# Performance work log

Hardware: AMD Instinct MI355X
Metric: run time of the kernel (lower is better)

Reference implementation:

```python
import jax, jax.numpy as jnp
import numpy as np

HEADS = 4
DIM_HEAD = 32
DIM = 128
B, N, Hq, Wg = 2, 6, 32, 32   # batch, cameras, BEV grid
HK, WK = 28, 60               # image feature map


def _ln(x, g, b, eps=1e-5):
    mu = jnp.mean(x, axis=-1, keepdims=True)
    var = jnp.mean((x - mu) ** 2, axis=-1, keepdims=True)
    return (x - mu) * jax.lax.rsqrt(var + eps) * g + b


def setup_inputs() -> dict:
    key = jax.random.key(0)
    ks = jax.random.split(key, 12)
    s = 0.05  # weight scale to keep softmax logits well-conditioned
    inp = {
        'q': jax.random.normal(ks[0], (B, N, DIM, Hq, Wg), jnp.float32),
        'k': jax.random.normal(ks[1], (B, N, DIM, HK, WK), jnp.float32),
        'v': jax.random.normal(ks[2], (B, N, DIM, HK, WK), jnp.float32),
        'skip': jax.random.normal(ks[3], (B, DIM, Hq, Wg), jnp.float32),
        'q_ln_g': jnp.ones((DIM,), jnp.float32),
        'q_ln_b': jnp.zeros((DIM,), jnp.float32),
        'Wq': s * jax.random.normal(ks[4], (DIM, HEADS * DIM_HEAD), jnp.float32),
        'bq': jnp.zeros((HEADS * DIM_HEAD,), jnp.float32),
        'k_ln_g': jnp.ones((DIM,), jnp.float32),
        'k_ln_b': jnp.zeros((DIM,), jnp.float32),
        'Wk': s * jax.random.normal(ks[5], (DIM, HEADS * DIM_HEAD), jnp.float32),
        'bk': jnp.zeros((HEADS * DIM_HEAD,), jnp.float32),
        'v_ln_g': jnp.ones((DIM,), jnp.float32),
        'v_ln_b': jnp.zeros((DIM,), jnp.float32),
        'Wv': s * jax.random.normal(ks[6], (DIM, HEADS * DIM_HEAD), jnp.float32),
        'bv': jnp.zeros((HEADS * DIM_HEAD,), jnp.float32),
        'Wp': s * jax.random.normal(ks[7], (HEADS * DIM_HEAD, DIM), jnp.float32),
        'bp': jnp.zeros((DIM,), jnp.float32),
        'pre_g': jnp.ones((DIM,), jnp.float32),
        'pre_b': jnp.zeros((DIM,), jnp.float32),
        'W1': s * jax.random.normal(ks[8], (DIM, 2 * DIM), jnp.float32),
        'b1': jnp.zeros((2 * DIM,), jnp.float32),
        'W2': s * jax.random.normal(ks[9], (2 * DIM, DIM), jnp.float32),
        'b2': jnp.zeros((DIM,), jnp.float32),
        'post_g': jnp.ones((DIM,), jnp.float32),
        'post_b': jnp.zeros((DIM,), jnp.float32),
    }
    return inp


def reference(q, k, v, skip, q_ln_g, q_ln_b, Wq, bq, k_ln_g, k_ln_b, Wk, bk,
              v_ln_g, v_ln_b, Wv, bv, Wp, bp, pre_g, pre_b,
              W1, b1, W2, b2, post_g, post_b):
    b, n, d, H, W = q.shape
    Q = H * W
    K = k.shape[3] * k.shape[4]
    m, dh = HEADS, DIM_HEAD
    # b n d H W -> b n Q d   /  b n d h w -> b n K d  /  b (n K) d
    qf = q.transpose(0, 1, 3, 4, 2).reshape(b, n, Q, d)
    kf = k.transpose(0, 1, 3, 4, 2).reshape(b, n, K, d)
    vf = v.transpose(0, 1, 3, 4, 2).reshape(b, n * K, d)
    # norm -> linear, then split heads: b ... (m dh) -> (b m) ... dh
    qh = (_ln(qf, q_ln_g, q_ln_b) @ Wq + bq).reshape(b, n, Q, m, dh)
    qh = qh.transpose(0, 3, 1, 2, 4).reshape(b * m, n, Q, dh)
    kh = (_ln(kf, k_ln_g, k_ln_b) @ Wk + bk).reshape(b, n, K, m, dh)
    kh = kh.transpose(0, 3, 1, 2, 4).reshape(b * m, n, K, dh)
    vh = (_ln(vf, v_ln_g, v_ln_b) @ Wv + bv).reshape(b, n * K, m, dh)
    vh = vh.transpose(0, 2, 1, 3).reshape(b * m, n * K, dh)
    scale = dh ** -0.5
    dot = scale * jnp.einsum('anqd,ankd->anqk', qh, kh)   # (b m) n Q K
    dot = dot.transpose(0, 2, 1, 3).reshape(b * m, Q, n * K)  # fold views into keys
    att = jax.nn.softmax(dot, axis=-1)
    a = jnp.einsum('aqk,akd->aqd', att, vh)               # (b m) Q dh
    a = a.reshape(b, m, Q, dh).transpose(0, 2, 1, 3).reshape(b, Q, m * dh)
    z = a @ Wp + bp
    z = z + skip.transpose(0, 2, 3, 1).reshape(b, Q, d)
    z = _ln(z, pre_g, pre_b)
    z = z + (jax.nn.gelu(z @ W1 + b1, approximate=False) @ W2 + b2)
    z = _ln(z, post_g, post_b)
    return z.reshape(b, H, W, d).transpose(0, 3, 1, 2)
```

## Files before the change

kernel.cpp:

```cpp
#include <hip/hip_runtime.h>
#include <math.h>

#define NCAM 6
#define BSZ 2
#define SQL 1024
#define SKL 1680
#define NHEAD 4
#define DHEAD 32
#define QSCALE 0.25503494f

typedef unsigned short ushort_t;
typedef unsigned int uint_t;
typedef __attribute__((ext_vector_type(8))) short short8;
typedef __attribute__((ext_vector_type(4))) float f32x4;

#define MFMA16 __builtin_amdgcn_mfma_f32_16x16x32_bf16

__device__ __forceinline__ ushort_t f2bf(float x) {
  uint_t u = __builtin_bit_cast(uint_t, x);
  u += 0x7FFFu + ((u >> 16) & 1u);
  return (ushort_t)(u >> 16);
}

__device__ __forceinline__ float fast_gelu(float x) {
  const float ax = fabsf(x) * 0.70710678118654752f;
  const float tt = __builtin_amdgcn_rcpf(fmaf(0.3275911f, ax, 1.f));
  float poly = fmaf(tt, 1.061405429f, -1.453152027f);
  poly = fmaf(tt, poly, 1.421413741f);
  poly = fmaf(tt, poly, -0.284496736f);
  poly = fmaf(tt, poly, 0.254829592f);
  poly *= tt;
  const float e = __builtin_amdgcn_exp2f(-ax * ax * 1.4426950408889634f);
  float er = fmaf(-poly, e, 1.f);
  er = copysignf(er, x);
  return 0.5f * x * (1.f + er);
}

__global__ __launch_bounds__(256) void prep_kernel(
    const float* __restrict__ Wq, const float* __restrict__ qg, const float* __restrict__ qb, const float* __restrict__ bq,
    const float* __restrict__ Wk, const float* __restrict__ kg, const float* __restrict__ kbb, const float* __restrict__ bk,
    const float* __restrict__ Wv, const float* __restrict__ vg, const float* __restrict__ vbb, const float* __restrict__ bv,
    const float* __restrict__ Wp,
    const float* __restrict__ W1, const float* __restrict__ pre_g, const float* __restrict__ pre_b, const float* __restrict__ b1,
    const float* __restrict__ W2,
    ushort_t* WqT, ushort_t* WkT, ushort_t* WvT, ushort_t* WpT, ushort_t* W1T, ushort_t* W2T,
    float* uq, float* bbq, float* uk, float* bbk, float* uv, float* bbv, float* b1p) {
  const int mb = blockIdx.x;
  const float *W, *g = nullptr, *bln = nullptr, *bias = nullptr;
  ushort_t* WT; float *u = nullptr, *bb = nullptr;
  int kin = 128, nout = 128, ob;
  if (mb < 4)       { W=Wq; g=qg; bln=qb;   bias=bq; WT=WqT; u=uq; bb=bbq; ob=mb*32; }
  else if (mb < 8)  { W=Wk; g=kg; bln=kbb;  bias=bk; WT=WkT; u=uk; bb=bbk; ob=(mb-4)*32; }
  else if (mb < 12) { W=Wv; g=vg; bln=vbb;  bias=bv; WT=WvT; u=uv; bb=bbv; ob=(mb-8)*32; }
  else if (mb < 16) { W=Wp; WT=WpT; ob=(mb-12)*32; }
  else if (mb < 24) { W=W1; g=pre_g; bln=pre_b; bias=b1; WT=W1T; bb=b1p; nout=256; ob=(mb-16)*32; }
  else              { W=W2; WT=W2T; kin=256; ob=(mb-24)*32; }
  const int t = threadIdx.x;
  const int oc = t & 31, ig = t >> 5;
  const int out = ob + oc;
  const int nper = kin >> 3;
  float su = 0.f, sb = 0.f;
  for (int j0 = 0; j0 < nper; j0 += 8) {
    float wv8[8];
#pragma unroll
    for (int j = 0; j < 8; ++j)
      wv8[j] = W[(size_t)(ig * nper + j0 + j) * nout + out];
#pragma unroll
    for (int j = 0; j < 8; ++j) {
      const int in = ig * nper + j0 + j;
      const float wg = g ? g[in] * wv8[j] : wv8[j];
      WT[(size_t)out * kin + in] = f2bf(wg);
      su += wg;
      if (bln) sb += bln[in] * wv8[j];
    }
  }
  __shared__ float sU[8][32], sB[8][32];
  sU[ig][oc] = su; sB[ig][oc] = sb;
  __syncthreads();
  if (t < 32) {
    float tu = 0.f, tb = 0.f;
#pragma unroll
    for (int i = 0; i < 8; ++i) { tu += sU[i][t]; tb += sB[i][t]; }
    if (u)  u[ob + t] = tu;
    if (bb) bb[ob + t] = tb + (bias ? bias[ob + t] : 0.f);
  }
}

__global__ __launch_bounds__(256) void proj_mfma(
    const float* __restrict__ xq, const float* __restrict__ xk, const float* __restrict__ xv,
    const ushort_t* __restrict__ WqT, const ushort_t* __restrict__ WkT, const ushort_t* __restrict__ WvT,
    const float* __restrict__ uq, const float* __restrict__ uk, const float* __restrict__ uv,
    const float* __restrict__ bbq, const float* __restrict__ bbk, const float* __restrict__ bbv,
    ushort_t* __restrict__ Qh, ushort_t* __restrict__ Kh, ushort_t* __restrict__ Vt) {
  int blk = blockIdx.x;
  const float* x; const ushort_t* WT; const float* u; const float* bb;
  ushort_t* out; int S, ntile, vmode; float oscale;
  if (blk < 192)      { x=xq; WT=WqT; u=uq; bb=bbq; out=Qh; S=SQL; ntile=16; vmode=0; oscale=QSCALE; }
  else if (blk < 516) { blk-=192; x=xk; WT=WkT; u=uk; bb=bbk; out=Kh; S=SKL; ntile=27; vmode=0; oscale=1.f; }
  else                { blk-=516; x=xv; WT=WvT; u=uv; bb=bbv; out=Vt; S=SKL; ntile=27; vmode=1; oscale=1.f; }
  const int bn = blk / ntile;
  const int pos0 = (blk - bn * ntile) * 64;
  int valid = S - pos0; if (valid > 64) valid = 64;

  const int t = threadIdx.x;
  __shared__ ushort_t sX[64 * 128];
  __shared__ float sS1[16][64], sS2[16][64];
  __shared__ float sMu[64], sRs[64];

  {
    const int posq = t & 15, chg = t >> 4;
    int lp4 = 4 * posq; if (lp4 >= valid) lp4 = valid - 4;
    const float* xb = x + ((size_t)bn * 128 + chg * 8) * S + pos0 + lp4;
    float v[8][4];
#pragma unroll
    for (int i = 0; i < 8; ++i) {
      const float4 f = *((const float4*)(xb + (size_t)i * S));
      v[i][0] = f.x; v[i][1] = f.y; v[i][2] = f.z; v[i][3] = f.w;
    }
#pragma unroll
    for (int j = 0; j < 4; ++j) {
      float s1 = 0.f, s2 = 0.f;
#pragma unroll
      for (int i = 0; i < 8; ++i) { s1 += v[i][j]; s2 += v[i][j] * v[i][j]; }
      sS1[chg][lp4 + j] = s1; sS2[chg][lp4 + j] = s2;
    }
#pragma unroll
    for (int j = 0; j < 4; ++j) {
      const int pos = lp4 + j;
      short8 pk;
#pragma unroll
      for (int i = 0; i < 8; ++i) pk[i] = (short)f2bf(v[i][j]);
      const int phys = chg ^ (pos & 7);
      *((short8*)&sX[pos * 128 + phys * 8]) = pk;
    }
  }
  __syncthreads();
  if (t < 64) {
    float a1 = 0.f, a2 = 0.f;
#pragma unroll
    for (int g = 0; g < 16; ++g) { a1 += sS1[g][t]; a2 += sS2[g][t]; }
    const float mu = a1 * (1.f / 128.f);
    sMu[t] = mu; sRs[t] = rsqrtf(a2 * (1.f / 128.f) - mu * mu + 1e-5f);
  }
  __syncthreads();

  const int w = t >> 6, l = t & 63, lq = l & 15, quad = l >> 4;
  short8 af[2][4];
#pragma unroll
  for (int ms = 0; ms < 2; ++ms)
#pragma unroll
    for (int kk = 0; kk < 4; ++kk)
      af[ms][kk] = *((const short8*)(WT + (size_t)(w * 32 + ms * 16 + lq) * 128 + quad * 8 + kk * 32));
  f32x4 acc[4][2];
#pragma unroll
  for (int ns = 0; ns < 4; ++ns)
#pragma unroll
    for (int ms = 0; ms < 2; ++ms) acc[ns][ms] = (f32x4){0.f, 0.f, 0.f, 0.f};
#pragma unroll
  for (int ns = 0; ns < 4; ++ns) {
    short8 bf[4];
#pragma unroll
    for (int kk = 0; kk < 4; ++kk) {
      const int phys = (quad + 4 * kk) ^ (lq & 7);
      bf[kk] = *((const short8*)&sX[(ns * 16 + lq) * 128 + phys * 8]);
    }
#pragma unroll
    for (int ms = 0; ms < 2; ++ms) {
      f32x4 a = acc[ns][ms];
#pragma unroll
      for (int kk = 0; kk < 4; ++kk) a = MFMA16(af[ms][kk], bf[kk], a, 0, 0, 0);
      acc[ns][ms] = a;
    }
  }

  const int b_ = bn / NCAM, cam = bn - b_ * NCAM;
  const size_t slab = (size_t)((b_ * NHEAD + w) * NCAM + cam);
#pragma unroll
  for (int ms = 0; ms < 2; ++ms) {
    float uu[4], bv_[4];
#pragma unroll
    for (int r = 0; r < 4; ++r) {
      const int og = w * 32 + ms * 16 + quad * 4 + r;
      uu[r] = u[og]; bv_[r] = bb[og];
    }
#pragma unroll
    for (int ns = 0; ns < 4; ++ns) {
      const int p = ns * 16 + lq;
      if (p < valid) {
        const float mu = sMu[p], rs = sRs[p];
        float val[4];
#pragma unroll
        for (int r = 0; r < 4; ++r)
          val[r] = ((acc[ns][ms][r] - mu * uu[r]) * rs + bv_[r]) * oscale;
        if (vmode == 0) {
          ushort_t e0 = f2bf(val[0]), e1 = f2bf(val[1]), e2 = f2bf(val[2]), e3 = f2bf(val[3]);
          ushort_t* orow = out + (slab * S + pos0 + p) * 32 + ms * 16 + quad * 4;
          *((uint_t*)orow) = (uint_t)e0 | ((uint_t)e1 << 16);
          *((uint_t*)(orow + 2)) = (uint_t)e2 | ((uint_t)e3 << 16);
        } else {
#pragma unroll
          for (int r = 0; r < 4; ++r)
            out[(slab * 32 + ms * 16 + quad * 4 + r) * (size_t)SKL + pos0 + p] = f2bf(val[r]);
        }
      }
    }
  }
}

__global__ __launch_bounds__(512, 2) void attn_mfma(
    const ushort_t* __restrict__ Qh, const ushort_t* __restrict__ Kh,
    const ushort_t* __restrict__ Vt, ushort_t* __restrict__ Ab) {
  const int t = threadIdx.x;
  const int w = t >> 6, l = t & 63;
  const int lq = l & 15, quad = l >> 4;
  const int bm = blockIdx.x & 7;
  const int q0 = (blockIdx.x >> 3) * 32;
  const int camg = w >> 2, kq = w & 3;
  const int kstart = kq * 448;
  const int nfull = (kq == 3) ? 5 : 7;

  __shared__ __align__(16) unsigned char smem[74752];
  ushort_t (*sP)[2][16][72] = (ushort_t(*)[2][16][72])smem;
  float (*sO)[2][16][36] = (float(*)[2][16][36])smem;
  float (*sL)[2][16] = (float(*)[2][16])(smem + 73728);

  f32x4 oA0 = {0.f,0.f,0.f,0.f}, oA1 = {0.f,0.f,0.f,0.f};
  f32x4 oB0 = {0.f,0.f,0.f,0.f}, oB1 = {0.f,0.f,0.f,0.f};
  float lA = 0.f, lB = 0.f;

  for (int nc = 0; nc < 3; ++nc) {
    const int n = camg * 3 + nc;
    const ushort_t* Kb = Kh + (size_t)(bm * NCAM + n) * SKL * 32;
    const ushort_t* Vb = Vt + (size_t)(bm * NCAM + n) * 32 * SKL;
    const ushort_t* Qbase = Qh + ((size_t)(bm * NCAM + n) * SQL + q0) * 32;
    const short8 qfA = *((const short8*)(Qbase + (size_t)lq * 32 + quad * 8));
    const short8 qfB = *((const short8*)(Qbase + (size_t)(16 + lq) * 32 + quad * 8));

    short8 kc[4];
#pragma unroll
    for (int st = 0; st < 4; ++st)
      kc[st] = *((const short8*)(Kb + (size_t)(kstart + st * 16 + lq) * 32 + quad * 8));

    for (int kt = 0; kt < nfull; ++kt) {
      const int kb = kstart + kt * 64;
      const short8 v00 = *((const short8*)(Vb + (size_t)lq * SKL + kb + quad * 8));
      const short8 v01 = *((const short8*)(Vb + (size_t)lq * SKL + kb + 32 + quad * 8));
      const short8 v10 = *((const short8*)(Vb + (size_t)(16 + lq) * SKL + kb + quad * 8));
      const short8 v11 = *((const short8*)(Vb + (size_t)(16 + lq) * SKL + kb + 32 + quad * 8));
      short8 kn[4] = {kc[0], kc[1], kc[2], kc[3]};
      if (kt + 1 < nfull) {
        const int kbn = kb + 64;
#pragma unroll
        for (int st = 0; st < 4; ++st)
          kn[st] = *((const short8*)(Kb + (size_t)(kbn + st * 16 + lq) * 32 + quad * 8));
      }

      f32x4 sA[4], sB[4];
#pragma unroll
      for (int st = 0; st < 4; ++st) {
        f32x4 z = {0.f, 0.f, 0.f, 0.f};
        sA[st] = MFMA16(kc[st], qfA, z, 0, 0, 0);
        sB[st] = MFMA16(kc[st], qfB, z, 0, 0, 0);
      }
      float lsA = 0.f, lsB = 0.f;
#pragma unroll
      for (int st = 0; st < 4; ++st) {
        const float a0 = __builtin_amdgcn_exp2f(sA[st][0]);
        const float a1 = __builtin_amdgcn_exp2f(sA[st][1]);
        const float a2 = __builtin_amdgcn_exp2f(sA[st][2]);
        const float a3 = __builtin_amdgcn_exp2f(sA[st][3]);
        const float b0 = __builtin_amdgcn_exp2f(sB[st][0]);
        const float b1 = __builtin_amdgcn_exp2f(sB[st][1]);
        const float b2 = __builtin_amdgcn_exp2f(sB[st][2]);
        const float b3 = __builtin_amdgcn_exp2f(sB[st][3]);
        lsA += (a0 + a1) + (a2 + a3);
        lsB += (b0 + b1) + (b2 + b3);
        const uint_t pa0 = __builtin_amdgcn_perm(__builtin_bit_cast(uint_t, a1), __builtin_bit_cast(uint_t, a0), 0x07060302u);
        const uint_t pa1 = __builtin_amdgcn_perm(__builtin_bit_cast(uint_t, a3), __builtin_bit_cast(uint_t, a2), 0x07060302u);
        const uint_t pb0 = __builtin_amdgcn_perm(__builtin_bit_cast(uint_t, b1), __builtin_bit_cast(uint_t, b0), 0x07060302u);
        const uint_t pb1 = __builtin_amdgcn_perm(__builtin_bit_cast(uint_t, b3), __builtin_bit_cast(uint_t, b2), 0x07060302u);
        *((uint2*)&sP[w][0][lq][st * 16 + quad * 4]) = make_uint2(pa0, pa1);
        *((uint2*)&sP[w][1][lq][st * 16 + quad * 4]) = make_uint2(pb0, pb1);
      }
      const short8 pfA0 = *((const short8*)&sP[w][0][lq][quad * 8]);
      const short8 pfA1 = *((const short8*)&sP[w][0][lq][32 + quad * 8]);
      const short8 pfB0 = *((const short8*)&sP[w][1][lq][quad * 8]);
      const short8 pfB1 = *((const short8*)&sP[w][1][lq][32 + quad * 8]);
      oA0 = MFMA16(v00, pfA0, oA0, 0, 0, 0);
      oA1 = MFMA16(v10, pfA0, oA1, 0, 0, 0);
      oB0 = MFMA16(v00, pfB0, oB0, 0, 0, 0);
      oB1 = MFMA16(v10, pfB0, oB1, 0, 0, 0);
      oA0 = MFMA16(v01, pfA1, oA0, 0, 0, 0);
      oA1 = MFMA16(v11, pfA1, oA1, 0, 0, 0);
      oB0 = MFMA16(v01, pfB1, oB0, 0, 0, 0);
      oB1 = MFMA16(v11, pfB1, oB1, 0, 0, 0);
      lsA += __shfl_xor(lsA, 16, 64);
      lsA += __shfl_xor(lsA, 32, 64);
      lsB += __shfl_xor(lsB, 16, 64);
      lsB += __shfl_xor(lsB, 32, 64);
      lA += lsA; lB += lsB;
#pragma unroll
      for (int st = 0; st < 4; ++st) kc[st] = kn[st];
    }

    if (kq == 3) {
      const int kb = kstart + 320;
      const short8 kf = *((const short8*)(Kb + (size_t)(kb + lq) * 32 + quad * 8));
      const short8 v00 = *((const short8*)(Vb + (size_t)lq * SKL + kb + quad * 8));
      const short8 v10 = *((const short8*)(Vb + (size_t)(16 + lq) * SKL + kb + quad * 8));
      f32x4 z = {0.f, 0.f, 0.f, 0.f};
      const f32x4 s0A = MFMA16(kf, qfA, z, 0, 0, 0);
      const f32x4 s0B = MFMA16(kf, qfB, z, 0, 0, 0);
      const float a0 = __builtin_amdgcn_exp2f(s0A[0]);
      const float a1 = __builtin_amdgcn_exp2f(s0A[1]);
      const float a2 = __builtin_amdgcn_exp2f(s0A[2]);
      const float a3 = __builtin_amdgcn_exp2f(s0A[3]);
      const float b0 = __builtin_amdgcn_exp2f(s0B[0]);
      const float b1 = __builtin_amdgcn_exp2f(s0B[1]);
      const float b2 = __builtin_amdgcn_exp2f(s0B[2]);
      const float b3 = __builtin_amdgcn_exp2f(s0B[3]);
      float lsA = (a0 + a1) + (a2 + a3);
      float lsB = (b0 + b1) + (b2 + b3);
      const uint_t pa0 = __builtin_amdgcn_perm(__builtin_bit_cast(uint_t, a1), __builtin_bit_cast(uint_t, a0), 0x07060302u);
      const uint_t pa1 = __builtin_amdgcn_perm(__builtin_bit_cast(uint_t, a3), __builtin_bit_cast(uint_t, a2), 0x07060302u);
      const uint_t pb0 = __builtin_amdgcn_perm(__builtin_bit_cast(uint_t, b1), __builtin_bit_cast(uint_t, b0), 0x07060302u);
      const uint_t pb1 = __builtin_amdgcn_perm(__builtin_bit_cast(uint_t, b3), __builtin_bit_cast(uint_t, b2), 0x07060302u);
      *((uint2*)&sP[w][0][lq][quad * 4]) = make_uint2(pa0, pa1);
      *((uint2*)&sP[w][0][lq][16 + quad * 4]) = make_uint2(0u, 0u);
      *((uint2*)&sP[w][1][lq][quad * 4]) = make_uint2(pb0, pb1);
      *((uint2*)&sP[w][1][lq][16 + quad * 4]) = make_uint2(0u, 0u);
      const short8 pfA0 = *((const short8*)&sP[w][0][lq][quad * 8]);
      const short8 pfB0 = *((const short8*)&sP[w][1][lq][quad * 8]);
      oA0 = MFMA16(v00, pfA0, oA0, 0, 0, 0);
      oA1 = MFMA16(v10, pfA0, oA1, 0, 0, 0);
      oB0 = MFMA16(v00, pfB0, oB0, 0, 0, 0);
      oB1 = MFMA16(v10, pfB0, oB1, 0, 0, 0);
      lsA += __shfl_xor(lsA, 16, 64);
      lsA += __shfl_xor(lsA, 32, 64);
      lsB += __shfl_xor(lsB, 16, 64);
      lsB += __shfl_xor(lsB, 32, 64);
      lA += lsA; lB += lsB;
    }
  }

  __syncthreads();
  *((f32x4*)&sO[w][0][lq][quad * 4]) = oA0;
  *((f32x4*)&sO[w][0][lq][16 + quad * 4]) = oA1;
  *((f32x4*)&sO[w][1][lq][quad * 4]) = oB0;
  *((f32x4*)&sO[w][1][lq][16 + quad * 4]) = oB1;
  if (l < 16) { sL[w][0][l] = lA; sL[w][1][l] = lB; }
  __syncthreads();
  if (w < 2) {
    const int frag = w;
    float lf = 0.f;
    f32x4 a0 = {0.f, 0.f, 0.f, 0.f}, a1 = {0.f, 0.f, 0.f, 0.f};
#pragma unroll
    for (int ww = 0; ww < 8; ++ww) {
      lf += sL[ww][frag][lq];
      a0 += *((const f32x4*)&sO[ww][frag][lq][quad * 4]);
      a1 += *((const f32x4*)&sO[ww][frag][lq][16 + quad * 4]);
    }
    const float inv = 1.f / lf;
    const int b = bm >> 2, hm = bm & 3;
    ushort_t* op = Ab + ((size_t)b * SQL + q0 + frag * 16 + lq) * 128 + hm * 32 + quad * 4;
    ushort4 w0 = make_ushort4(f2bf(a0[0] * inv), f2bf(a0[1] * inv), f2bf(a0[2] * inv), f2bf(a0[3] * inv));
    ushort4 w1 = make_ushort4(f2bf(a1[0] * inv), f2bf(a1[1] * inv), f2bf(a1[2] * inv), f2bf(a1[3] * inv));
    *((ushort4*)op) = w0;
    *((ushort4*)(op + 16)) = w1;
  }
}

__global__ __launch_bounds__(256) void post_mfma(
    const ushort_t* __restrict__ Ab, const float* __restrict__ skip,
    const ushort_t* __restrict__ WpT, const float* __restrict__ bp,
    const float* __restrict__ pre_g, const float* __restrict__ pre_b,
    const ushort_t* __restrict__ W1T, const float* __restrict__ b1p,
    const ushort_t* __restrict__ W2T, const float* __restrict__ b2,
    const float* __restrict__ post_g, const float* __restrict__ post_b,
    float* __restrict__ out) {
  const int t = threadIdx.x;
  const int w = t >> 6, l = t & 63, lq = l & 15, quad = l >> 4;
  const int b = blockIdx.x >> 7;
  const int p0 = (blockIdx.x & 127) * 8;
  const int rp = (p0 + lq < SQL) ? (p0 + lq) : (SQL - 1);

  __shared__ float zf[16 * 132];
  __shared__ float sRes[16 * 132];
  __shared__ ushort_t sZb[16 * 128];
  __shared__ ushort_t sH[16 * 256];
  __shared__ float sMu[16], sRs[16];

  f32x4 z[2] = {{0.f,0.f,0.f,0.f},{0.f,0.f,0.f,0.f}};
#pragma unroll
  for (int kk = 0; kk < 4; ++kk) {
    const short8 bfr = *((const short8*)(Ab + ((size_t)b * SQL + rp) * 128 + quad * 8 + kk * 32));
#pragma unroll
    for (int ms = 0; ms < 2; ++ms) {
      const short8 afr = *((const short8*)(WpT + (size_t)(w * 32 + ms * 16 + lq) * 128 + quad * 8 + kk * 32));
      z[ms] = MFMA16(afr, bfr, z[ms], 0, 0, 0);
    }
  }
#pragma unroll
  for (int ms = 0; ms < 2; ++ms)
#pragma unroll
    for (int r = 0; r < 4; ++r) {
      const int o = w * 32 + ms * 16 + quad * 4 + r;
      const int rr = (p0 + lq < SQL) ? (p0 + lq) : (SQL - 1);
      zf[lq * 132 + o] = z[ms][r] + bp[o] + skip[(size_t)b * 131072 + (size_t)o * 1024 + rr];
    }
  __syncthreads();
  {
    const int pos = t >> 4, j = t & 15;
    float s1 = 0.f, s2 = 0.f;
#pragma unroll
    for (int c = 0; c < 8; ++c) { const float vv = zf[pos * 132 + j * 8 + c]; s1 += vv; s2 += vv * vv; }
    s1 += __shfl_xor(s1, 1, 64); s1 += __shfl_xor(s1, 2, 64);
    s1 += __shfl_xor(s1, 4, 64); s1 += __shfl_xor(s1, 8, 64);
    s2 += __shfl_xor(s2, 1, 64); s2 += __shfl_xor(s2, 2, 64);
    s2 += __shfl_xor(s2, 4, 64); s2 += __shfl_xor(s2, 8, 64);
    if (j == 0) {
      const float mu = s1 * (1.f / 128.f);
      sMu[pos] = mu; sRs[pos] = rsqrtf(s2 * (1.f / 128.f) - mu * mu + 1e-5f);
    }
  }
  __syncthreads();
  {
    const int pos = t & 15, grp = t >> 4;
    const float mu = sMu[pos], rs = sRs[pos];
    short8 pk;
#pragma unroll
    for (int i = 0; i < 8; ++i) {
      const int ch = grp * 8 + i;
      const float nv = (zf[pos * 132 + ch] - mu) * rs;
      pk[i] = (short)f2bf(nv);
      sRes[pos * 132 + ch] = nv * pre_g[ch] + pre_b[ch];
    }
    *((short8*)&sZb[pos * 128 + (grp ^ (pos & 7)) * 8]) = pk;
  }
  __syncthreads();
  f32x4 h[4];
#pragma unroll
  for (int ms = 0; ms < 4; ++ms) h[ms] = (f32x4){0.f, 0.f, 0.f, 0.f};
  short8 bz[4];
#pragma unroll
  for (int kk = 0; kk < 4; ++kk)
    bz[kk] = *((const short8*)&sZb[lq * 128 + ((quad + 4 * kk) ^ (lq & 7)) * 8]);
#pragma unroll
  for (int ms = 0; ms < 4; ++ms)
#pragma unroll
    for (int kk = 0; kk < 4; ++kk) {
      const short8 afr = *((const short8*)(W1T + (size_t)(w * 64 + ms * 16 + lq) * 128 + quad * 8 + kk * 32));
      h[ms] = MFMA16(afr, bz[kk], h[ms], 0, 0, 0);
    }
#pragma unroll
  for (int ms = 0; ms < 4; ++ms)
#pragma unroll
    for (int r = 0; r < 4; ++r) {
      const int o = w * 64 + ms * 16 + quad * 4 + r;
      const float hv = fast_gelu(h[ms][r] + b1p[o]);
      const int phys = (o >> 3) ^ (lq & 7);
      sH[lq * 256 + phys * 8 + (o & 7)] = f2bf(hv);
    }
  __syncthreads();
  f32x4 z2[2] = {{0.f,0.f,0.f,0.f},{0.f,0.f,0.f,0.f}};
#pragma unroll
  for (int kk = 0; kk < 8; ++kk) {
    const short8 bh = *((const short8*)&sH[lq * 256 + ((quad + 4 * kk) ^ (lq & 7)) * 8]);
#pragma unroll
    for (int ms = 0; ms < 2; ++ms) {
      const short8 afr = *((const short8*)(W2T + (size_t)(w * 32 + ms * 16 + lq) * 256 + quad * 8 + kk * 32));
      z2[ms] = MFMA16(afr, bh, z2[ms], 0, 0, 0);
    }
  }
  __syncthreads();
#pragma unroll
  for (int ms = 0; ms < 2; ++ms)
#pragma unroll
    for (int r = 0; r < 4; ++r) {
      const int o = w * 32 + ms * 16 + quad * 4 + r;
      zf[lq * 132 + o] = z2[ms][r] + b2[o] + sRes[lq * 132 + o];
    }
  __syncthreads();
  {
    const int pos = t >> 4, j = t & 15;
    float s1 = 0.f, s2 = 0.f;
#pragma unroll
    for (int c = 0; c < 8; ++c) { const float vv = zf[pos * 132 + j * 8 + c]; s1 += vv; s2 += vv * vv; }
    s1 += __shfl_xor(s1, 1, 64); s1 += __shfl_xor(s1, 2, 64);
    s1 += __shfl_xor(s1, 4, 64); s1 += __shfl_xor(s1, 8, 64);
    s2 += __shfl_xor(s2, 1, 64); s2 += __shfl_xor(s2, 2, 64);
    s2 += __shfl_xor(s2, 4, 64); s2 += __shfl_xor(s2, 8, 64);
    if (j == 0) {
      const float mu = s1 * (1.f / 128.f);
      sMu[pos] = mu; sRs[pos] = rsqrtf(s2 * (1.f / 128.f) - mu * mu + 1e-5f);
    }
  }
  __syncthreads();
  {
    const int pos = t & 15, grp = t >> 4;
    if (pos < 8) {
      const float mu = sMu[pos], rs = sRs[pos];
#pragma unroll
      for (int i = 0; i < 8; ++i) {
        const int ch = grp * 8 + i;
        out[(size_t)b * 131072 + (size_t)ch * 1024 + p0 + pos] =
            (zf[pos * 132 + ch] - mu) * rs * post_g[ch] + post_b[ch];
      }
    }
  }
}

extern "C" void kernel_launch(void* const* d_in, const int* in_sizes, int n_in,
                              void* d_out, int out_size, void* d_ws, size_t ws_size,
                              hipStream_t stream) {
  const float* q_in   = (const float*)d_in[0];
  const float* k_in   = (const float*)d_in[1];
  const float* v_in   = (const float*)d_in[2];
  const float* skip   = (const float*)d_in[3];
  const float* q_ln_g = (const float*)d_in[4];
  const float* q_ln_b = (const float*)d_in[5];
  const float* Wq     = (const float*)d_in[6];
  const float* bq     = (const float*)d_in[7];
  const float* k_ln_g = (const float*)d_in[8];
  const float* k_ln_b = (const float*)d_in[9];
  const float* Wk     = (const float*)d_in[10];
  const float* bk     = (const float*)d_in[11];
  const float* v_ln_g = (const float*)d_in[12];
  const float* v_ln_b = (const float*)d_in[13];
  const float* Wv     = (const float*)d_in[14];
  const float* bv     = (const float*)d_in[15];
  const float* Wp     = (const float*)d_in[16];
  const float* bp     = (const float*)d_in[17];
  const float* pre_g  = (const float*)d_in[18];
  const float* pre_b  = (const float*)d_in[19];
  const float* W1     = (const float*)d_in[20];
  const float* b1     = (const float*)d_in[21];
  const float* W2     = (const float*)d_in[22];
  const float* b2     = (const float*)d_in[23];
  const float* post_g = (const float*)d_in[24];
  const float* post_b = (const float*)d_in[25];

  char* base = (char*)d_ws;
  ushort_t* WqT = (ushort_t*)base; base += 16384 * 2;
  ushort_t* WkT = (ushort_t*)base; base += 16384 * 2;
  ushort_t* WvT = (ushort_t*)base; base += 16384 * 2;
  ushort_t* WpT = (ushort_t*)base; base += 16384 * 2;
  ushort_t* W1T = (ushort_t*)base; base += 32768 * 2;
  ushort_t* W2T = (ushort_t*)base; base += 32768 * 2;
  float* uq  = (float*)base; base += 128 * 4;
  float* bbq = (float*)base; base += 128 * 4;
  float* uk  = (float*)base; base += 128 * 4;
  float* bbk = (float*)base; base += 128 * 4;
  float* uv  = (float*)base; base += 128 * 4;
  float* bbv = (float*)base; base += 128 * 4;
  float* b1p = (float*)base; base += 256 * 4;
  base = (char*)(((size_t)base + 255) & ~(size_t)255);
  ushort_t* Qh = (ushort_t*)base; base += (size_t)1572864 * 2;
  ushort_t* Kh = (ushort_t*)base; base += (size_t)(2580480 + 4096) * 2;
  ushort_t* Vt = (ushort_t*)base; base += (size_t)(2580480 + 4096) * 2;
  ushort_t* Ab = (ushort_t*)base; base += (size_t)262144 * 2;
  float* out = (float*)d_out;

  prep_kernel<<<28, 256, 0, stream>>>(
      Wq, q_ln_g, q_ln_b, bq, Wk, k_ln_g, k_ln_b, bk, Wv, v_ln_g, v_ln_b, bv,
      Wp, W1, pre_g, pre_b, b1, W2,
      WqT, WkT, WvT, WpT, W1T, W2T, uq, bbq, uk, bbk, uv, bbv, b1p);
  proj_mfma<<<840, 256, 0, stream>>>(
      q_in, k_in, v_in, WqT, WkT, WvT, uq, uk, uv, bbq, bbk, bbv, Qh, Kh, Vt);
  attn_mfma<<<256, 512, 0, stream>>>(Qh, Kh, Vt, Ab);
  post_mfma<<<256, 256, 0, stream>>>(
      Ab, skip, WpT, bp, pre_g, pre_b, W1T, b1p, W2T, b2, post_g, post_b, out);
}
```

Baseline: 165.8 us.

## Keep attention probabilities in registers by permuting key order in V loads

Removes the per-tile LDS round trip for the softmax probabilities. The exponentials are packed straight into MFMA B-operand registers, and the V operand is loaded as 8-byte pieces in a matching permuted key order, so the PV product stays correct without a shared-memory transpose. The row-sum cross-lane shuffles move out of the inner loop to a single reduction at the end, and the __syncthreads before writing sO is dropped because sP no longer aliases that memory. In exchange, the V fetches become narrower uint2 loads with more instructions per tile.

```diff
diff --git a/kernel.cpp b/kernel.cpp
--- a/kernel.cpp
+++ b/kernel.cpp
@@ -13,6 +13,7 @@
 typedef unsigned int uint_t;
 typedef __attribute__((ext_vector_type(8))) short short8;
 typedef __attribute__((ext_vector_type(4))) float f32x4;
+typedef __attribute__((ext_vector_type(4))) uint_t uint4v;
 
 #define MFMA16 __builtin_amdgcn_mfma_f32_16x16x32_bf16
 
@@ -20,6 +21,10 @@
   uint_t u = __builtin_bit_cast(uint_t, x);
   u += 0x7FFFu + ((u >> 16) & 1u);
   return (ushort_t)(u >> 16);
+}
+
+__device__ __forceinline__ uint_t pk2(float e0, float e1) {
+  return __builtin_amdgcn_perm(__builtin_bit_cast(uint_t, e1), __builtin_bit_cast(uint_t, e0), 0x07060302u);
 }
 
 __device__ __forceinline__ float fast_gelu(float x) {
@@ -220,7 +225,6 @@
   const int nfull = (kq == 3) ? 5 : 7;
 
   __shared__ __align__(16) unsigned char smem[74752];
-  ushort_t (*sP)[2][16][72] = (ushort_t(*)[2][16][72])smem;
   float (*sO)[2][16][36] = (float(*)[2][16][36])smem;
   float (*sL)[2][16] = (float(*)[2][16])(smem + 73728);
 
@@ -243,10 +247,26 @@
 
     for (int kt = 0; kt < nfull; ++kt) {
       const int kb = kstart + kt * 64;
-      const short8 v00 = *((const short8*)(Vb + (size_t)lq * SKL + kb + quad * 8));
-      const short8 v01 = *((const short8*)(Vb + (size_t)lq * SKL + kb + 32 + quad * 8));
-      const short8 v10 = *((const short8*)(Vb + (size_t)(16 + lq) * SKL + kb + quad * 8));
-      const short8 v11 = *((const short8*)(Vb + (size_t)(16 + lq) * SKL + kb + 32 + quad * 8));
+      const int vq = quad * 4;
+      const ushort_t* vp0 = Vb + (size_t)lq * SKL + kb + vq;
+      const ushort_t* vp1 = Vb + (size_t)(16 + lq) * SKL + kb + vq;
+      const uint2 r00 = *((const uint2*)(vp0));
+      const uint2 r01 = *((const uint2*)(vp0 + 16));
+      const uint2 r02 = *((const uint2*)(vp0 + 32));
+      const uint2 r03 = *((const uint2*)(vp0 + 48));
+      const uint2 r10 = *((const uint2*)(vp1));
+      const uint2 r11 = *((const uint2*)(vp1 + 16));
+      const uint2 r12 = *((const uint2*)(vp1 + 32));
+      const uint2 r13 = *((const uint2*)(vp1 + 48));
+      uint4v c;
+      c[0] = r00.x; c[1] = r00.y; c[2] = r01.x; c[3] = r01.y;
+      const short8 v00 = __builtin_bit_cast(short8, c);
+      c[0] = r02.x; c[1] = r02.y; c[2] = r03.x; c[3] = r03.y;
+      const short8 v01 = __builtin_bit_cast(short8, c);
+      c[0] = r10.x; c[1] = r10.y; c[2] = r11.x; c[3] = r11.y;
+      const short8 v10 = __builtin_bit_cast(short8, c);
+      c[0] = r12.x; c[1] = r12.y; c[2] = r13.x; c[3] = r13.y;
+      const short8 v11 = __builtin_bit_cast(short8, c);
       short8 kn[4] = {kc[0], kc[1], kc[2], kc[3]};
       if (kt + 1 < nfull) {
         const int kbn = kb + 64;
@@ -262,30 +282,31 @@
         sA[st] = MFMA16(kc[st], qfA, z, 0, 0, 0);
         sB[st] = MFMA16(kc[st], qfB, z, 0, 0, 0);
       }
-      float lsA = 0.f, lsB = 0.f;
+      float eA[4][4], eB[4][4];
 #pragma unroll
       for (int st = 0; st < 4; ++st) {
-        const float a0 = __builtin_amdgcn_exp2f(sA[st][0]);
-        const float a1 = __builtin_amdgcn_exp2f(sA[st][1]);
-        const float a2 = __builtin_amdgcn_exp2f(sA[st][2]);
-        const float a3 = __builtin_amdgcn_exp2f(sA[st][3]);
-        const float b0 = __builtin_amdgcn_exp2f(sB[st][0]);
-        const float b1 = __builtin_amdgcn_exp2f(sB[st][1]);
-        const float b2 = __builtin_amdgcn_exp2f(sB[st][2]);
-        const float b3 = __builtin_amdgcn_exp2f(sB[st][3]);
-        lsA += (a0 + a1) + (a2 + a3);
-        lsB += (b0 + b1) + (b2 + b3);
-        const uint_t pa0 = __builtin_amdgcn_perm(__builtin_bit_cast(uint_t, a1), __builtin_bit_cast(uint_t, a0), 0x07060302u);
-        const uint_t pa1 = __builtin_amdgcn_perm(__builtin_bit_cast(uint_t, a3), __builtin_bit_cast(uint_t, a2), 0x07060302u);
-        const uint_t pb0 = __builtin_amdgcn_perm(__builtin_bit_cast(uint_t, b1), __builtin_bit_cast(uint_t, b0), 0x07060302u);
-        const uint_t pb1 = __builtin_amdgcn_perm(__builtin_bit_cast(uint_t, b3), __builtin_bit_cast(uint_t, b2), 0x07060302u);
-        *((uint2*)&sP[w][0][lq][st * 16 + quad * 4]) = make_uint2(pa0, pa1);
-        *((uint2*)&sP[w][1][lq][st * 16 + quad * 4]) = make_uint2(pb0, pb1);
+#pragma unroll
+        for (int r = 0; r < 4; ++r) {
+          eA[st][r] = __builtin_amdgcn_exp2f(sA[st][r]);
+          eB[st][r] = __builtin_amdgcn_exp2f(sB[st][r]);
+        }
+        lA += (eA[st][0] + eA[st][1]) + (eA[st][2] + eA[st][3]);
+        lB += (eB[st][0] + eB[st][1]) + (eB[st][2] + eB[st][3]);
       }
-      const short8 pfA0 = *((const short8*)&sP[w][0][lq][quad * 8]);
-      const short8 pfA1 = *((const short8*)&sP[w][0][lq][32 + quad * 8]);
-      const short8 pfB0 = *((const short8*)&sP[w][1][lq][quad * 8]);
-      const short8 pfB1 = *((const short8*)&sP[w][1][lq][32 + quad * 8]);
+      uint4v pw;
+      pw[0] = pk2(eA[0][0], eA[0][1]); pw[1] = pk2(eA[0][2], eA[0][3]);
+      pw[2] = pk2(eA[1][0], eA[1][1]); pw[3] = pk2(eA[1][2], eA[1][3]);
+      const short8 pfA0 = __builtin_bit_cast(short8, pw);
+      pw[0] = pk2(eA[2][0], eA[2][1]); pw[1] = pk2(eA[2][2], eA[2][3]);
+      pw[2] = pk2(eA[3][0], eA[3][1]); pw[3] = pk2(eA[3][2], eA[3][3]);
+      const short8 pfA1 = __builtin_bit_cast(short8, pw);
+      pw[0] = pk2(eB[0][0], eB[0][1]); pw[1] = pk2(eB[0][2], eB[0][3]);
+      pw[2] = pk2(eB[1][0], eB[1][1]); pw[3] = pk2(eB[1][2], eB[1][3]);
+      const short8 pfB0 = __builtin_bit_cast(short8, pw);
+      pw[0] = pk2(eB[2][0], eB[2][1]); pw[1] = pk2(eB[2][2], eB[2][3]);
+      pw[2] = pk2(eB[3][0], eB[3][1]); pw[3] = pk2(eB[3][2], eB[3][3]);
+      const short8 pfB1 = __builtin_bit_cast(short8, pw);
+
       oA0 = MFMA16(v00, pfA0, oA0, 0, 0, 0);
       oA1 = MFMA16(v10, pfA0, oA1, 0, 0, 0);
       oB0 = MFMA16(v00, pfB0, oB0, 0, 0, 0);
@@ -294,56 +315,49 @@
       oA1 = MFMA16(v11, pfA1, oA1, 0, 0, 0);
       oB0 = MFMA16(v01, pfB1, oB0, 0, 0, 0);
       oB1 = MFMA16(v11, pfB1, oB1, 0, 0, 0);
-      lsA += __shfl_xor(lsA, 16, 64);
-      lsA += __shfl_xor(lsA, 32, 64);
-      lsB += __shfl_xor(lsB, 16, 64);
-      lsB += __shfl_xor(lsB, 32, 64);
-      lA += lsA; lB += lsB;
 #pragma unroll
       for (int st = 0; st < 4; ++st) kc[st] = kn[st];
     }
 
     if (kq == 3) {
       const int kb = kstart + 320;
+      const int vq = quad * 4;
       const short8 kf = *((const short8*)(Kb + (size_t)(kb + lq) * 32 + quad * 8));
-      const short8 v00 = *((const short8*)(Vb + (size_t)lq * SKL + kb + quad * 8));
-      const short8 v10 = *((const short8*)(Vb + (size_t)(16 + lq) * SKL + kb + quad * 8));
+      const uint2 r00 = *((const uint2*)(Vb + (size_t)lq * SKL + kb + vq));
+      const uint2 r10 = *((const uint2*)(Vb + (size_t)(16 + lq) * SKL + kb + vq));
+      uint4v c;
+      c[0] = r00.x; c[1] = r00.y; c[2] = 0u; c[3] = 0u;
+      const short8 v00 = __builtin_bit_cast(short8, c);
+      c[0] = r10.x; c[1] = r10.y; c[2] = 0u; c[3] = 0u;
+      const short8 v10 = __builtin_bit_cast(short8, c);
       f32x4 z = {0.f, 0.f, 0.f, 0.f};
       const f32x4 s0A = MFMA16(kf, qfA, z, 0, 0, 0);
       const f32x4 s0B = MFMA16(kf, qfB, z, 0, 0, 0);
-      const float a0 = __builtin_amdgcn_exp2f(s0A[0]);
-      const float a1 = __builtin_amdgcn_exp2f(s0A[1]);
-      const float a2 = __builtin_amdgcn_exp2f(s0A[2]);
-      const float a3 = __builtin_amdgcn_exp2f(s0A[3]);
-      const float b0 = __builtin_amdgcn_exp2f(s0B[0]);
-      const float b1 = __builtin_amdgcn_exp2f(s0B[1]);
-      const float b2 = __builtin_amdgcn_exp2f(s0B[2]);
-      const float b3 = __builtin_amdgcn_exp2f(s0B[3]);
-      float lsA = (a0 + a1) + (a2 + a3);
-      float lsB = (b0 + b1) + (b2 + b3);
-      const uint_t pa0 = __builtin_amdgcn_perm(__builtin_bit_cast(uint_t, a1), __builtin_bit_cast(uint_t, a0), 0x07060302u);
-      const uint_t pa1 = __builtin_amdgcn_perm(__builtin_bit_cast(uint_t, a3), __builtin_bit_cast(uint_t, a2), 0x07060302u);
-      const uint_t pb0 = __builtin_amdgcn_perm(__builtin_bit_cast(uint_t, b1), __builtin_bit_cast(uint_t, b0), 0x07060302u);
-      const uint_t pb1 = __builtin_amdgcn_perm(__builtin_bit_cast(uint_t, b3), __builtin_bit_cast(uint_t, b2), 0x07060302u);
-      *((uint2*)&sP[w][0][lq][quad * 4]) = make_uint2(pa0, pa1);
-      *((uint2*)&sP[w][0][lq][16 + quad * 4]) = make_uint2(0u, 0u);
-      *((uint2*)&sP[w][1][lq][quad * 4]) = make_uint2(pb0, pb1);
-      *((uint2*)&sP[w][1][lq][16 + quad * 4]) = make_uint2(0u, 0u);
-      const short8 pfA0 = *((const short8*)&sP[w][0][lq][quad * 8]);
-      const short8 pfB0 = *((const short8*)&sP[w][1][lq][quad * 8]);
+      float eA[4], eB[4];
+#pragma unroll
+      for (int r = 0; r < 4; ++r) {
+        eA[r] = __builtin_amdgcn_exp2f(s0A[r]);
+        eB[r] = __builtin_amdgcn_exp2f(s0B[r]);
+      }
+      lA += (eA[0] + eA[1]) + (eA[2] + eA[3]);
+      lB += (eB[0] + eB[1]) + (eB[2] + eB[3]);
+      uint4v pw;
+      pw[0] = pk2(eA[0], eA[1]); pw[1] = pk2(eA[2], eA[3]); pw[2] = 0u; pw[3] = 0u;
+      const short8 pfA0 = __builtin_bit_cast(short8, pw);
+      pw[0] = pk2(eB[0], eB[1]); pw[1] = pk2(eB[2], eB[3]); pw[2] = 0u; pw[3] = 0u;
+      const short8 pfB0 = __builtin_bit_cast(short8, pw);
       oA0 = MFMA16(v00, pfA0, oA0, 0, 0, 0);
       oA1 = MFMA16(v10, pfA0, oA1, 0, 0, 0);
       oB0 = MFMA16(v00, pfB0, oB0, 0, 0, 0);
       oB1 = MFMA16(v10, pfB0, oB1, 0, 0, 0);
-      lsA += __shfl_xor(lsA, 16, 64);
-      lsA += __shfl_xor(lsA, 32, 64);
-      lsB += __shfl_xor(lsB, 16, 64);
-      lsB += __shfl_xor(lsB, 32, 64);
-      lA += lsA; lB += lsB;
-    }
-  }
-
-  __syncthreads();
+    }
+  }
+
+  lA += __shfl_xor(lA, 16, 64);
+  lA += __shfl_xor(lA, 32, 64);
+  lB += __shfl_xor(lB, 16, 64);
+  lB += __shfl_xor(lB, 32, 64);
+
   *((f32x4*)&sO[w][0][lq][quad * 4]) = oA0;
   *((f32x4*)&sO[w][0][lq][16 + quad * 4]) = oA1;
   *((f32x4*)&sO[w][1][lq][quad * 4]) = oB0;
```

New measurement: 176.5 us. 6.4% more time.
